# Kernel tuning notes

Hardware: AMD Instinct MI355X
Metric: run time of the kernel (lower is better)

## Reference

```python
import jax, jax.numpy as jnp
import numpy as np

SIDE = 64; EMB = 16; CH = 64; K = 64; V = 64; L = 8
N = SIDE * SIDE

def _pos_table(side, d):
    pe = np.array([[p / np.power(10000, 2 * (j // 2) / d) for j in range(d)]
                   if p != 0 else np.zeros(d) for p in range(side)])
    pe[1:, 0::2] = np.sin(pe[1:, 0::2])
    pe[1:, 1::2] = np.cos(pe[1:, 1::2])
    return pe.astype(np.float32)  # [side, d]

def _pos_emb():
    # Replicates torch .view(1, emb, side, 1): plain reshape of [side, emb] -> [emb, side]
    t = _pos_table(SIDE, EMB).reshape(EMB, SIDE)
    xe = np.broadcast_to(t[:, :, None], (EMB, SIDE, SIDE))
    ye = np.broadcast_to(t[:, None, :], (EMB, SIDE, SIDE))
    return jnp.asarray(np.concatenate([xe, ye], 0).reshape(1, 2 * EMB, N))

def _conv_mask():
    # CausalConv mask, see_center=False, 5x5: zero center pixel onward in center row, and all rows below
    m = np.ones((CH, 3, 5, 5), np.float32)
    m[:, :, 2, 2:] = 0.0
    m[:, :, 3:, :] = 0.0
    return jnp.asarray(m)

def _lrelu(x):
    return jnp.where(x >= 0, x, 0.01 * x)  # LeakyReLU(0.01)

def _bn(x, g, b, eps=1e-5):
    # training-mode batch norm (biased variance), channel axis = 1
    axes = (0,) + tuple(range(2, x.ndim))
    m = jnp.mean(x, axes, keepdims=True)
    var = jnp.mean((x - m) ** 2, axes, keepdims=True)
    sh = (1, -1) + (1,) * (x.ndim - 2)
    return g.reshape(sh) * (x - m) / jnp.sqrt(var + eps) + b.reshape(sh)

def _cv1(w, b, x):
    # 1x1 Conv1d: [O,I] x [B,I,N] -> [B,O,N]
    return jnp.einsum('oi,bin->bon', w, x) + b[:, None]

def reference(x, conv_w, conv_b, bn0_g, bn0_b, q_w, q_b, fk_w, fk_b, ck_w, ck_b,
              fv_w, fv_b, cv_w, cv_b, bn_g, bn_b, out_w, out_b):
    B = x.shape[0]
    pos = jnp.broadcast_to(_pos_emb(), (B, 2 * EMB, N))
    mask = jnp.tril(jnp.ones((N, N), jnp.float32))

    # masked causal conv input layer + BN + LeakyReLU
    w = conv_w * _conv_mask()
    h = jax.lax.conv_general_dilated(x, w, (1, 1), [(2, 2), (2, 2)],
                                     dimension_numbers=('NCHW', 'OIHW', 'NCHW'))
    h = h + conv_b[None, :, None, None]
    h = _lrelu(_bn(h, bn0_g, bn0_b)).reshape(B, CH, N)

    k0 = jnp.zeros((B, K, N), x.dtype)
    v0 = jnp.zeros((B, V, N), x.dtype)
    inv_sqrt_k = 1.0 / jnp.sqrt(jnp.float32(K))

    def layer(carry, p):
        h, k, v = carry
        qw, qb, fkw, fkb, ckw, ckb, fvw, fvb, cvw, cvb, g, bb = p
        x0 = jnp.concatenate([h, pos], 1)            # [B, CH+32, N]
        x0k = jnp.concatenate([x0, k], 1)            # [B, 160, N]
        x0v = jnp.concatenate([x0, v], 1)
        fk = jax.nn.sigmoid(_cv1(fkw, fkb, x0k))
        ck = _lrelu(_cv1(ckw, ckb, x0k))
        k_new = fk * k + ck                          # highway-gated persistent K
        fv = jax.nn.sigmoid(_cv1(fvw, fvb, x0v))
        cv_ = _lrelu(_cv1(cvw, cvb, x0v))
        v_new = fv * v + cv_
        q = _lrelu(_cv1(qw, qb, x0))                 # [B, K, N]
        attn = jnp.einsum('bkn,bkm->bnm', q, k) * inv_sqrt_k  # uses OLD k
        attn = attn * mask + (1.0 - mask) * (-10000.0)
        attn = jax.nn.softmax(attn, axis=-1) * mask
        out1 = jnp.einsum('bnm,bvm->bvn', attn, v)   # uses OLD v; [B, V, N]
        # original code computes fc(out1) but discards it (out2 overwritten)
        h2 = _lrelu(_bn(out1, g, bb))
        return (h2, k_new, v_new), None

    params = (q_w, q_b, fk_w, fk_b, ck_w, ck_b, fv_w, fv_b, cv_w, cv_b, bn_g, bn_b)
    (h, k, v), _ = jax.lax.scan(layer, (h, k0, v0), params)

    out = jnp.einsum('oi,bin->bon', out_w, h) + out_b[None, :, None]
    return out.reshape(B, out_w.shape[0], SIDE, SIDE)

def setup_inputs() -> dict:
    key = jax.random.key(0)
    ks = jax.random.split(key, 12)
    s = 0.05
    return {
        'x': jax.random.normal(ks[0], (2, 3, 64, 64), jnp.float32),
        'conv_w': jax.random.normal(ks[1], (CH, 3, 5, 5), jnp.float32) * s,
        'conv_b': jnp.zeros((CH,), jnp.float32),
        'bn0_g': jnp.ones((CH,), jnp.float32),
        'bn0_b': jnp.zeros((CH,), jnp.float32),
        'q_w': jax.random.normal(ks[2], (L, K, CH + 2 * EMB), jnp.float32) * s,
        'q_b': jnp.zeros((L, K), jnp.float32),
        'fk_w': jax.random.normal(ks[3], (L, K, CH + K + 2 * EMB), jnp.float32) * s,
        'fk_b': jnp.zeros((L, K), jnp.float32),
        'ck_w': jax.random.normal(ks[4], (L, K, CH + K + 2 * EMB), jnp.float32) * s,
        'ck_b': jnp.zeros((L, K), jnp.float32),
        'fv_w': jax.random.normal(ks[5], (L, V, CH + V + 2 * EMB), jnp.float32) * s,
        'fv_b': jnp.zeros((L, V), jnp.float32),
        'cv_w': jax.random.normal(ks[6], (L, V, CH + V + 2 * EMB), jnp.float32) * s,
        'cv_b': jnp.zeros((L, V), jnp.float32),
        'bn_g': jnp.ones((L, CH), jnp.float32),
        'bn_b': jnp.zeros((L, CH), jnp.float32),
        'out_w': jax.random.normal(ks[7], (100, V), jnp.float32) * s,
        'out_b': jnp.zeros((100,), jnp.float32),
    }
```

## Files before the change

### kernel.cpp

```cpp
#include <hip/hip_runtime.h>

#define NPIX 4096
#define CHN  64

typedef __attribute__((ext_vector_type(8))) short short8;
typedef __attribute__((ext_vector_type(8))) unsigned short ushort8;
typedef __attribute__((ext_vector_type(4))) unsigned short ushort4v;
typedef __attribute__((ext_vector_type(4))) float f32x4;

__device__ __forceinline__ float lrelu_(float x){ return x >= 0.f ? x : 0.01f*x; }

__device__ __forceinline__ unsigned short f2bf(float x){
  union { float f; unsigned u; } v; v.f = x;
  unsigned r = v.u + 0x7FFF + ((v.u >> 16) & 1);
  return (unsigned short)(r >> 16);
}
__device__ __forceinline__ float bf2f(unsigned short h){
  union { unsigned u; float f; } v; v.u = ((unsigned)h) << 16;
  return v.f;
}

__global__ void pos_kernel(float* __restrict__ pos){
  int idx = blockIdx.x*256 + threadIdx.x;
  int c = idx >> 12;
  int n = idx & (NPIX-1);
  int bcoord = (c < 16) ? (n >> 6) : (n & 63);
  int a = (c < 16) ? c : (c - 16);
  int flat = a*64 + bcoord;
  int p = flat >> 4;
  int j = flat & 15;
  float val = 0.f;
  if (p != 0){
    float ex = (float)(j & ~1) * (1.f/16.f);
    float w = powf(10000.f, -ex);
    float ang = (float)p * w;
    val = (j & 1) ? cosf(ang) : sinf(ang);
  }
  pos[idx] = val;
}

__global__ void wtr_kernel(const float* __restrict__ qw, const float* __restrict__ fkw,
                           const float* __restrict__ ckw, const float* __restrict__ fvw,
                           const float* __restrict__ cvw, float* __restrict__ wt){
  int idx = blockIdx.x*256 + threadIdx.x;
  if (idx >= 376832) return;
  if (idx < 49152){
    int l = idx / 6144, r = idx % 6144, i = r >> 6, o = r & 63;
    wt[idx] = qw[(l*64 + o)*96 + i];
  } else {
    int e = idx - 49152;
    int mat = e / 81920, r = e % 81920;
    int l = r / 10240, rr = r % 10240, i = rr >> 6, o = rr & 63;
    const float* src = (mat==0) ? fkw : (mat==1) ? ckw : (mat==2) ? fvw : cvw;
    wt[idx] = src[(l*64 + o)*160 + i];
  }
}

__global__ void conv_in_kernel(const float* __restrict__ x, const float* __restrict__ cw,
                               const float* __restrict__ cb, float* __restrict__ out){
  int b = blockIdx.x >> 6;
  int o = blockIdx.x & 63;
  float w[3][12];
  #pragma unroll
  for (int ci=0; ci<3; ++ci){
    const float* wp = cw + (o*3+ci)*25;
    #pragma unroll
    for (int tt=0; tt<10; ++tt) w[ci][tt] = wp[tt];
    w[ci][10] = wp[10]; w[ci][11] = wp[11];
  }
  float bias = cb[o];
  for (int px = threadIdx.x; px < NPIX; px += 256){
    int y = px >> 6, xx = px & 63;
    float acc = bias;
    #pragma unroll
    for (int ci=0; ci<3; ++ci){
      const float* xp = x + ((b*3+ci)<<12);
      #pragma unroll
      for (int ky=0; ky<3; ++ky){
        int yy = y + ky - 2;
        if (yy < 0) continue;
        int nk = (ky==2) ? 2 : 5;
        #pragma unroll
        for (int kx=0; kx<5; ++kx){
          if (kx >= nk) break;
          int xc = xx + kx - 2;
          if (xc < 0 || xc > 63) continue;
          acc += xp[(yy<<6) + xc] * w[ci][ky*5+kx];
        }
      }
    }
    out[(b*CHN+o)*NPIX + px] = acc;
  }
}

__global__ __launch_bounds__(1024) void bn_stats_kernel(const float* __restrict__ xin,
                                                        float* __restrict__ stats){
  int c = blockIdx.x;
  int t = threadIdx.x;
  float s = 0.f, ss = 0.f;
  #pragma unroll
  for (int it=0; it<8; ++it){
    int idx = t + it*1024;
    float v = xin[(((idx>>12))*CHN + c)*NPIX + (idx & (NPIX-1))];
    s += v; ss += v*v;
  }
  #pragma unroll
  for (int o=1; o<64; o<<=1){ s += __shfl_xor(s,o); ss += __shfl_xor(ss,o); }
  __shared__ float ps[16], pq[16];
  if ((t & 63) == 0){ ps[t>>6] = s; pq[t>>6] = ss; }
  __syncthreads();
  if (t == 0){
    float S=0.f, Q=0.f;
    #pragma unroll
    for (int i=0;i<16;++i){ S += ps[i]; Q += pq[i]; }
    float mu = S*(1.f/8192.f);
    float var = Q*(1.f/8192.f) - mu*mu;
    var = fmaxf(var, 0.f);
    stats[c*2]   = mu;
    stats[c*2+1] = rsqrtf(var + 1e-5f);
  }
}

__global__ void bn_apply_kernel(const float* __restrict__ xin, const float* __restrict__ stats,
                                const float* __restrict__ g, const float* __restrict__ bb,
                                float* __restrict__ hout){
  int idx = blockIdx.x*256 + threadIdx.x;
  int e = idx << 2;
  int c = (e >> 12) & 63;
  float mu = stats[c*2], rstd = stats[c*2+1];
  float gain = g[c]*rstd;
  float beta = bb[c] - gain*mu;
  float4 v = *(const float4*)(xin + e);
  float4 r;
  r.x = lrelu_(gain*v.x + beta);
  r.y = lrelu_(gain*v.y + beta);
  r.z = lrelu_(gain*v.z + beta);
  r.w = lrelu_(gain*v.w + beta);
  *(float4*)(hout + e) = r;
}

__global__ __launch_bounds__(256) void cv1_kernel(
    const float* __restrict__ hbuf, const float* __restrict__ pos,
    const float* __restrict__ kold, const float* __restrict__ vold,
    const float* __restrict__ qwt,
    const float* __restrict__ fkwt, const float* __restrict__ ckwt,
    const float* __restrict__ fvwt, const float* __restrict__ cvwt,
    const float* __restrict__ qbi,  const float* __restrict__ fkb,
    const float* __restrict__ ckb,  const float* __restrict__ fvb,
    const float* __restrict__ cvb,
    unsigned short* __restrict__ qh, unsigned short* __restrict__ ql,
    float* __restrict__ knew, unsigned short* __restrict__ khn, unsigned short* __restrict__ kln,
    float* __restrict__ vnew, unsigned short* __restrict__ vhTn, unsigned short* __restrict__ vlTn)
{
  int t = threadIdx.x;
  int o  = t & 63;
  int wv = t >> 6;
  int b    = blockIdx.x >> 8;
  int tile = blockIdx.x & 255;
  int n0 = tile*16 + wv*4;

  const float* hb = hbuf + b*CHN*NPIX + n0;
  const float* kb = kold + b*CHN*NPIX + n0;
  const float* vb = vold + b*CHN*NPIX + n0;
  const float* pb = pos + n0;

  auto load4 = [&](const float* p, float* dst){
    float4 a = *(const float4*)p;
    dst[0]=a.x; dst[1]=a.y; dst[2]=a.z; dst[3]=a.w;
  };

  float x[4];
  long obase = (long)(b*CHN+o)*NPIX + n0;
  size_t nbase = ((size_t)b*NPIX + n0)*64 + o;

  {
    float aq[4];
    float bias = qbi[o];
    #pragma unroll
    for (int j=0;j<4;++j) aq[j]=bias;
    #pragma unroll 4
    for (int i=0;i<64;++i){
      load4(hb + i*NPIX, x);
      float w = qwt[i*64 + o];
      #pragma unroll
      for (int j=0;j<4;++j) aq[j] += w*x[j];
    }
    #pragma unroll 4
    for (int i=0;i<32;++i){
      load4(pb + i*NPIX, x);
      float w = qwt[(64+i)*64 + o];
      #pragma unroll
      for (int j=0;j<4;++j) aq[j] += w*x[j];
    }
    #pragma unroll
    for (int j=0;j<4;++j){
      float v = lrelu_(aq[j]) * 0.125f;
      unsigned short hb16 = f2bf(v);
      qh[nbase + (size_t)j*64] = hb16;
      ql[nbase + (size_t)j*64] = f2bf(v - bf2f(hb16));
    }
  }

  {
    float af[4], ac[4];
    float bf = fkb[o], bc = ckb[o];
    #pragma unroll
    for (int j=0;j<4;++j){ af[j]=bf; ac[j]=bc; }
    #pragma unroll 4
    for (int i=0;i<64;++i){
      load4(hb + i*NPIX, x);
      float wf = fkwt[i*64+o], wc = ckwt[i*64+o];
      #pragma unroll
      for (int j=0;j<4;++j){ af[j] += wf*x[j]; ac[j] += wc*x[j]; }
    }
    #pragma unroll 4
    for (int i=0;i<32;++i){
      load4(pb + i*NPIX, x);
      float wf = fkwt[(64+i)*64+o], wc = ckwt[(64+i)*64+o];
      #pragma unroll
      for (int j=0;j<4;++j){ af[j] += wf*x[j]; ac[j] += wc*x[j]; }
    }
    #pragma unroll 4
    for (int i=0;i<64;++i){
      load4(kb + i*NPIX, x);
      float wf = fkwt[(96+i)*64+o], wc = ckwt[(96+i)*64+o];
      #pragma unroll
      for (int j=0;j<4;++j){ af[j] += wf*x[j]; ac[j] += wc*x[j]; }
    }
    float kv[4];
    load4(kb + o*NPIX, kv);
    #pragma unroll
    for (int j=0;j<4;++j){
      float fk = 1.f/(1.f+__expf(-af[j]));
      float kn = fk*kv[j] + lrelu_(ac[j]);
      knew[obase+j] = kn;
      unsigned short hb16 = f2bf(kn);
      khn[nbase + (size_t)j*64] = hb16;
      kln[nbase + (size_t)j*64] = f2bf(kn - bf2f(hb16));
    }
  }

  {
    float af[4], ac[4];
    float bf = fvb[o], bc = cvb[o];
    #pragma unroll
    for (int j=0;j<4;++j){ af[j]=bf; ac[j]=bc; }
    #pragma unroll 4
    for (int i=0;i<64;++i){
      load4(hb + i*NPIX, x);
      float wf = fvwt[i*64+o], wc = cvwt[i*64+o];
      #pragma unroll
      for (int j=0;j<4;++j){ af[j] += wf*x[j]; ac[j] += wc*x[j]; }
    }
    #pragma unroll 4
    for (int i=0;i<32;++i){
      load4(pb + i*NPIX, x);
      float wf = fvwt[(64+i)*64+o], wc = cvwt[(64+i)*64+o];
      #pragma unroll
      for (int j=0;j<4;++j){ af[j] += wf*x[j]; ac[j] += wc*x[j]; }
    }
    #pragma unroll 4
    for (int i=0;i<64;++i){
      load4(vb + i*NPIX, x);
      float wf = fvwt[(96+i)*64+o], wc = cvwt[(96+i)*64+o];
      #pragma unroll
      for (int j=0;j<4;++j){ af[j] += wf*x[j]; ac[j] += wc*x[j]; }
    }
    float vv[4];
    load4(vb + o*NPIX, vv);
    ushort4v vph, vpl;
    #pragma unroll
    for (int j=0;j<4;++j){
      float fv = 1.f/(1.f+__expf(-af[j]));
      float vn = fv*vv[j] + lrelu_(ac[j]);
      vnew[obase+j] = vn;
      unsigned short hb16 = f2bf(vn);
      vph[j] = hb16;
      vpl[j] = f2bf(vn - bf2f(hb16));
    }
    *(ushort4v*)(vhTn + ((size_t)(b*CHN+o))*NPIX + n0) = vph;
    *(ushort4v*)(vlTn + ((size_t)(b*CHN+o))*NPIX + n0) = vpl;
  }
}

__global__ __launch_bounds__(128) void attn_mfma(
    const unsigned short* __restrict__ qhg, const unsigned short* __restrict__ qlg,
    const unsigned short* __restrict__ khg, const unsigned short* __restrict__ klg,
    const unsigned short* __restrict__ vhg, const unsigned short* __restrict__ vlg,
    float* __restrict__ part)
{
  int bid = 639 - (int)blockIdx.x;
  int b = 0, id = bid;
  if (id >= 320){ b = 1; id -= 320; }
  int pidx = bid;
  int rem = id, k = 0;
  while (rem >= 32*(k+1)){ rem -= 32*(k+1); ++k; }
  int rt    = 32*k + rem/(k+1);
  int chunk = rem - (rem/(k+1))*(k+1);

  int C0  = chunk << 10;
  int end = min(C0 + 1024, rt*32 + 32);
  int nt  = (end - C0 + 63) >> 6;

  int t = threadIdx.x;
  int w = t >> 6;
  int l = t & 63;
  int r = l & 15;
  int g = l >> 4;
  int n_g = rt*32 + w*16 + r;

  __shared__ __align__(16) char KH[8192], KL[8192];
  __shared__ __align__(16) char VH[8192], VL[8192];
  __shared__ __align__(16) char PH[2][2048], PL[2][2048];

  const unsigned short* qhp = qhg + (size_t)b*NPIX*64;
  const unsigned short* qlp = qlg + (size_t)b*NPIX*64;
  const unsigned short* khp = khg + (size_t)b*NPIX*64;
  const unsigned short* klp = klg + (size_t)b*NPIX*64;
  const unsigned short* vhp = vhg + (size_t)b*CHN*NPIX;
  const unsigned short* vlp = vlg + (size_t)b*CHN*NPIX;

  short8 qh0 = *(const short8*)(qhp + (size_t)n_g*64 + 8*g);
  short8 qh1 = *(const short8*)(qhp + (size_t)n_g*64 + 8*g + 32);
  short8 ql0 = *(const short8*)(qlp + (size_t)n_g*64 + 8*g);
  short8 ql1 = *(const short8*)(qlp + (size_t)n_g*64 + 8*g + 32);

  f32x4 zero4 = {0.f,0.f,0.f,0.f};
  f32x4 oacc[4];
  #pragma unroll
  for (int vf=0; vf<4; ++vf) oacc[vf] = zero4;
  float m_run = -1e30f, l_run = 0.f;

  int nmax_w = rt*32 + w*16 + 15;

  for (int ti=0; ti<nt; ++ti){
    int m0 = C0 + (ti<<6);
    __syncthreads();
    #pragma unroll
    for (int p=0; p<4; ++p){
      int slot = t + (p<<7);
      int row = slot >> 3, cc = slot & 7;
      int off = row*128 + ((cc ^ (row & 7)) << 4);
      *(ushort8*)(KH + off) = *(const ushort8*)(khp + (size_t)(m0+row)*64 + cc*8);
      *(ushort8*)(KL + off) = *(const ushort8*)(klp + (size_t)(m0+row)*64 + cc*8);
      *(ushort8*)(VH + off) = *(const ushort8*)(vhp + (size_t)row*NPIX + m0 + cc*8);
      *(ushort8*)(VL + off) = *(const ushort8*)(vlp + (size_t)row*NPIX + m0 + cc*8);
    }
    __syncthreads();

    if (m0 <= nmax_w){
      f32x4 sf[4];
      #pragma unroll
      for (int mf=0; mf<4; ++mf) sf[mf] = zero4;
      #pragma unroll
      for (int kc=0; kc<2; ++kc){
        short8 qfh = kc ? qh1 : qh0;
        short8 qfl = kc ? ql1 : ql0;
        int ch = ((g + 4*kc) ^ (r & 7)) << 4;
        #pragma unroll
        for (int mf=0; mf<4; ++mf){
          int ro = (16*mf + r)*128;
          short8 ah = *(const short8*)(KH + ro + ch);
          short8 al = *(const short8*)(KL + ro + ch);
          sf[mf] = __builtin_amdgcn_mfma_f32_16x16x32_bf16(ah, qfh, sf[mf], 0,0,0);
          sf[mf] = __builtin_amdgcn_mfma_f32_16x16x32_bf16(al, qfh, sf[mf], 0,0,0);
          sf[mf] = __builtin_amdgcn_mfma_f32_16x16x32_bf16(ah, qfl, sf[mf], 0,0,0);
        }
      }
      float pv[16];
      float mx = -1e30f;
      #pragma unroll
      for (int mf=0; mf<4; ++mf){
        #pragma unroll
        for (int q2=0; q2<4; ++q2){
          int mg = m0 + 16*mf + 4*g + q2;
          float s = sf[mf][q2];
          s = (mg <= n_g) ? s : -1e30f;
          pv[mf*4+q2] = s;
          mx = fmaxf(mx, s);
        }
      }
      mx = fmaxf(mx, __shfl_xor(mx, 16));
      mx = fmaxf(mx, __shfl_xor(mx, 32));
      float m_new = fmaxf(m_run, mx);
      float alpha = __expf(m_run - m_new);
      float ps = 0.f;
      #pragma unroll
      for (int i=0; i<16; ++i){ pv[i] = __expf(pv[i] - m_new); ps += pv[i]; }
      ps += __shfl_xor(ps, 16);
      ps += __shfl_xor(ps, 32);
      l_run = l_run*alpha + ps;
      m_run = m_new;

      #pragma unroll
      for (int mf=0; mf<4; ++mf){
        unsigned short h_[4], l_[4];
        #pragma unroll
        for (int q2=0; q2<4; ++q2){
          float xv = pv[mf*4+q2];
          h_[q2] = f2bf(xv);
          l_[q2] = f2bf(xv - bf2f(h_[q2]));
        }
        int addr = r*128 + ((((g>>1) + 2*mf) ^ (r & 7)) << 4) + ((g&1)<<3);
        uint2 wh = make_uint2((unsigned)h_[0] | ((unsigned)h_[1]<<16),
                              (unsigned)h_[2] | ((unsigned)h_[3]<<16));
        uint2 wl = make_uint2((unsigned)l_[0] | ((unsigned)l_[1]<<16),
                              (unsigned)l_[2] | ((unsigned)l_[3]<<16));
        *(uint2*)(PH[w] + addr) = wh;
        *(uint2*)(PL[w] + addr) = wl;
      }
      #pragma unroll
      for (int vf=0; vf<4; ++vf) oacc[vf] *= alpha;

      #pragma unroll
      for (int kc=0; kc<2; ++kc){
        int ch = ((g + 4*kc) ^ (r & 7)) << 4;
        short8 pfh = *(const short8*)(PH[w] + r*128 + ch);
        short8 pfl = *(const short8*)(PL[w] + r*128 + ch);
        #pragma unroll
        for (int vf=0; vf<4; ++vf){
          int ro = (16*vf + r)*128;
          short8 ah = *(const short8*)(VH + ro + ch);
          short8 al = *(const short8*)(VL + ro + ch);
          oacc[vf] = __builtin_amdgcn_mfma_f32_16x16x32_bf16(ah, pfh, oacc[vf], 0,0,0);
          oacc[vf] = __builtin_amdgcn_mfma_f32_16x16x32_bf16(al, pfh, oacc[vf], 0,0,0);
          oacc[vf] = __builtin_amdgcn_mfma_f32_16x16x32_bf16(ah, pfl, oacc[vf], 0,0,0);
        }
      }
    }
  }

  float* pacc = part + (size_t)pidx * 2112;
  int nl = w*16 + r;
  #pragma unroll
  for (int vf=0; vf<4; ++vf)
    *(f32x4*)(pacc + nl*64 + 16*vf + 4*g) = oacc[vf];
  if (g == 0){
    pacc[2048 + nl*2]   = m_run;
    pacc[2048 + nl*2+1] = l_run;
  }
}

__global__ __launch_bounds__(256) void attn_combine(const float* __restrict__ part,
                                                    float* __restrict__ out1){
  int bid = blockIdx.x;
  int b = bid >> 7, rt = bid & 127;
  int k = rt >> 5;
  int nch = k + 1;
  int base = b*320 + 16*k*(k+1) + (rt - 32*k)*nch;

  int t = threadIdx.x;
  int nl = t & 31, vq = t >> 5;

  float M = -1e30f;
  #pragma unroll
  for (int c=0; c<4; ++c)
    if (c < nch) M = fmaxf(M, part[(size_t)(base+c)*2112 + 2048 + nl*2]);

  float L = 0.f;
  float val[8];
  #pragma unroll
  for (int jj=0; jj<8; ++jj) val[jj] = 0.f;
  #pragma unroll
  for (int c=0; c<4; ++c){
    if (c < nch){
      const float* pa = part + (size_t)(base+c)*2112;
      float wgt = __expf(pa[2048 + nl*2] - M);
      L += pa[2048 + nl*2 + 1] * wgt;
      #pragma unroll
      for (int jj=0; jj<8; ++jj) val[jj] += wgt * pa[nl*64 + vq*8 + jj];
    }
  }
  float invL = 1.f / L;
  #pragma unroll
  for (int jj=0; jj<8; ++jj)
    out1[((size_t)b*CHN + vq*8 + jj)*NPIX + rt*32 + nl] = val[jj]*invL;
}

__global__ __launch_bounds__(256) void final_kernel(const float* __restrict__ h,
                                                    const float* __restrict__ ow,
                                                    const float* __restrict__ ob,
                                                    float* __restrict__ out){
  int idx = blockIdx.x*256 + threadIdx.x;
  int b  = idx / 409600;
  int r  = idx - b*409600;
  int oc = r >> 12;
  int n  = r & (NPIX-1);
  const float* hp = h + (size_t)b*CHN*NPIX + n;
  const float* wp = ow + oc*64;
  float acc = ob[oc];
  #pragma unroll
  for (int v=0; v<64; ++v) acc += wp[v]*hp[(size_t)v*NPIX];
  out[idx] = acc;
}

extern "C" void kernel_launch(void* const* d_in, const int* in_sizes, int n_in,
                              void* d_out, int out_size, void* d_ws, size_t ws_size,
                              hipStream_t stream){
  const float* x     = (const float*)d_in[0];
  const float* convw = (const float*)d_in[1];
  const float* convb = (const float*)d_in[2];
  const float* bn0g  = (const float*)d_in[3];
  const float* bn0b  = (const float*)d_in[4];
  const float* qw    = (const float*)d_in[5];
  const float* qbias = (const float*)d_in[6];
  const float* fkw   = (const float*)d_in[7];
  const float* fkb   = (const float*)d_in[8];
  const float* ckw   = (const float*)d_in[9];
  const float* ckb   = (const float*)d_in[10];
  const float* fvw   = (const float*)d_in[11];
  const float* fvb   = (const float*)d_in[12];
  const float* cvw   = (const float*)d_in[13];
  const float* cvb   = (const float*)d_in[14];
  const float* bng   = (const float*)d_in[15];
  const float* bnb   = (const float*)d_in[16];
  const float* ow    = (const float*)d_in[17];
  const float* ob    = (const float*)d_in[18];

  const size_t TEN = (size_t)2*CHN*NPIX;
  const size_t BFU = TEN/2;
  float* ws   = (float*)d_ws;
  float* pos  = ws;
  float* h    = pos + 32*NPIX;
  float* k0   = h  + TEN;
  float* k1   = k0 + TEN;
  float* v0   = k1 + TEN;
  float* v1   = v0 + TEN;
  float* o1   = v1 + TEN;
  float* stats = o1 + TEN;
  float* wt   = stats + 128;
  float* bfb  = wt + 376832;
  unsigned short* qh  = (unsigned short*)(bfb);
  unsigned short* ql  = (unsigned short*)(bfb + BFU);
  unsigned short* kh0 = (unsigned short*)(bfb + 2*BFU);
  unsigned short* kh1 = (unsigned short*)(bfb + 3*BFU);
  unsigned short* kl0 = (unsigned short*)(bfb + 4*BFU);
  unsigned short* kl1 = (unsigned short*)(bfb + 5*BFU);
  unsigned short* vh0 = (unsigned short*)(bfb + 6*BFU);
  unsigned short* vh1 = (unsigned short*)(bfb + 7*BFU);
  unsigned short* vl0 = (unsigned short*)(bfb + 8*BFU);
  unsigned short* vl1 = (unsigned short*)(bfb + 9*BFU);
  float* part = bfb + 10*BFU;

  hipMemsetAsync(k0, 0, TEN*sizeof(float), stream);
  hipMemsetAsync(v0, 0, TEN*sizeof(float), stream);
  hipMemsetAsync(kh0, 0, TEN*2, stream);
  hipMemsetAsync(kl0, 0, TEN*2, stream);
  hipMemsetAsync(vh0, 0, TEN*2, stream);
  hipMemsetAsync(vl0, 0, TEN*2, stream);

  pos_kernel<<<512,256,0,stream>>>(pos);
  wtr_kernel<<<1472,256,0,stream>>>(qw, fkw, ckw, fvw, cvw, wt);
  conv_in_kernel<<<128,256,0,stream>>>(x, convw, convb, o1);
  bn_stats_kernel<<<64,1024,0,stream>>>(o1, stats);
  bn_apply_kernel<<<512,256,0,stream>>>(o1, stats, bn0g, bn0b, h);

  float* kfp[2] = {k0,k1};
  float* vfp[2] = {v0,v1};
  unsigned short* khb[2] = {kh0,kh1};
  unsigned short* klb[2] = {kl0,kl1};
  unsigned short* vhb[2] = {vh0,vh1};
  unsigned short* vlb[2] = {vl0,vl1};
  for (int l=0; l<8; ++l){
    float* kold = kfp[l&1]; float* knew = kfp[(l+1)&1];
    float* vold = vfp[l&1]; float* vnew = vfp[(l+1)&1];
    cv1_kernel<<<512,256,0,stream>>>(h, pos, kold, vold,
        wt + l*6144,
        wt + 49152 + l*10240,
        wt + 49152 + 81920 + l*10240,
        wt + 49152 + 2*81920 + l*10240,
        wt + 49152 + 3*81920 + l*10240,
        qbias + l*64, fkb + l*64, ckb + l*64, fvb + l*64, cvb + l*64,
        qh, ql,
        knew, khb[(l+1)&1], klb[(l+1)&1],
        vnew, vhb[(l+1)&1], vlb[(l+1)&1]);
    attn_mfma<<<640,128,0,stream>>>(qh, ql, khb[l&1], klb[l&1], vhb[l&1], vlb[l&1], part);
    attn_combine<<<256,256,0,stream>>>(part, o1);
    bn_stats_kernel<<<64,1024,0,stream>>>(o1, stats);
    bn_apply_kernel<<<512,256,0,stream>>>(o1, stats, bng + l*64, bnb + l*64, h);
  }
  final_kernel<<<3200,256,0,stream>>>(h, ow, ob, (float*)d_out);
}
```

Before: 869.2 us.

## Fuse BN stats into attention combine, prefetch attention tiles, parallelize input conv

Three separate changes. First, attn_combine now emits per-block partial sums and squared sums per channel, and a new bn_apply2 kernel reduces them, removing the separate bn_stats pass over o1 in every layer. Second, attn_mfma register-prefetches the next K/V tile from global memory while the current tile is being computed, overlapping load latency with MFMA work. Third, the input convolution weights are transposed in wtr_kernel and conv_in is launched with many more blocks, one pixel per thread group. The variance is now computed as E[x^2]-mu^2, which is less numerically robust than the two-pass form, and the prefetch adds register pressure.

```diff
diff --git a/kernel.cpp b/kernel.cpp
--- a/kernel.cpp
+++ b/kernel.cpp
@@ -41,56 +41,57 @@
 
 __global__ void wtr_kernel(const float* __restrict__ qw, const float* __restrict__ fkw,
                            const float* __restrict__ ckw, const float* __restrict__ fvw,
-                           const float* __restrict__ cvw, float* __restrict__ wt){
+                           const float* __restrict__ cvw, const float* __restrict__ convw,
+                           float* __restrict__ wt){
   int idx = blockIdx.x*256 + threadIdx.x;
-  if (idx >= 376832) return;
+  if (idx >= 381632) return;
   if (idx < 49152){
     int l = idx / 6144, r = idx % 6144, i = r >> 6, o = r & 63;
     wt[idx] = qw[(l*64 + o)*96 + i];
-  } else {
+  } else if (idx < 376832){
     int e = idx - 49152;
     int mat = e / 81920, r = e % 81920;
     int l = r / 10240, rr = r % 10240, i = rr >> 6, o = rr & 63;
     const float* src = (mat==0) ? fkw : (mat==1) ? ckw : (mat==2) ? fvw : cvw;
     wt[idx] = src[(l*64 + o)*160 + i];
-  }
-}
-
-__global__ void conv_in_kernel(const float* __restrict__ x, const float* __restrict__ cw,
-                               const float* __restrict__ cb, float* __restrict__ out){
-  int b = blockIdx.x >> 6;
-  int o = blockIdx.x & 63;
-  float w[3][12];
+  } else {
+    int e = idx - 376832;
+    int o = e & 63, tap = e >> 6;
+    int ci = tap / 25, r = tap % 25;
+    wt[idx] = convw[(o*3 + ci)*25 + r];
+  }
+}
+
+__global__ __launch_bounds__(256) void conv_in_kernel(const float* __restrict__ x,
+                                                      const float* __restrict__ cwt,
+                                                      const float* __restrict__ cb,
+                                                      float* __restrict__ out){
+  int t = threadIdx.x;
+  int o = t & 63;
+  int sub = t >> 6;
+  int bid = blockIdx.x;
+  int b = bid >> 10;
+  int n = ((bid & 1023) << 2) + sub;
+  int y = n >> 6, xx = n & 63;
+  float acc = cb[o];
   #pragma unroll
   for (int ci=0; ci<3; ++ci){
-    const float* wp = cw + (o*3+ci)*25;
-    #pragma unroll
-    for (int tt=0; tt<10; ++tt) w[ci][tt] = wp[tt];
-    w[ci][10] = wp[10]; w[ci][11] = wp[11];
-  }
-  float bias = cb[o];
-  for (int px = threadIdx.x; px < NPIX; px += 256){
-    int y = px >> 6, xx = px & 63;
-    float acc = bias;
-    #pragma unroll
-    for (int ci=0; ci<3; ++ci){
-      const float* xp = x + ((b*3+ci)<<12);
-      #pragma unroll
-      for (int ky=0; ky<3; ++ky){
-        int yy = y + ky - 2;
-        if (yy < 0) continue;
-        int nk = (ky==2) ? 2 : 5;
-        #pragma unroll
-        for (int kx=0; kx<5; ++kx){
-          if (kx >= nk) break;
-          int xc = xx + kx - 2;
-          if (xc < 0 || xc > 63) continue;
-          acc += xp[(yy<<6) + xc] * w[ci][ky*5+kx];
-        }
+    const float* xp = x + ((b*3+ci)<<12);
+    #pragma unroll
+    for (int ky=0; ky<3; ++ky){
+      int yy = y + ky - 2;
+      if (yy < 0) continue;
+      int nk = (ky==2) ? 2 : 5;
+      #pragma unroll
+      for (int kx=0; kx<5; ++kx){
+        if (kx >= nk) break;
+        int xc = xx + kx - 2;
+        if (xc < 0 || xc > 63) continue;
+        acc += xp[(yy<<6) + xc] * cwt[(ci*25 + ky*5 + kx)*64 + o];
       }
     }
-    out[(b*CHN+o)*NPIX + px] = acc;
-  }
+  }
+  out[(b*CHN+o)*NPIX + n] = acc;
 }
 
 __global__ __launch_bounds__(1024) void bn_stats_kernel(const float* __restrict__ xin,
@@ -137,6 +138,39 @@
   r.z = lrelu_(gain*v.z + beta);
   r.w = lrelu_(gain*v.w + beta);
   *(float4*)(hout + e) = r;
+}
+
+__global__ __launch_bounds__(256) void bn_apply2_kernel(const float* __restrict__ xin,
+                                                        const float* __restrict__ psum,
+                                                        const float* __restrict__ psq,
+                                                        const float* __restrict__ g,
+                                                        const float* __restrict__ bb,
+                                                        float* __restrict__ hout){
+  int bid = blockIdx.x;
+  int ebase = bid << 10;
+  int c = (ebase >> 12) & 63;
+  int t = threadIdx.x;
+  float s = psum[c*256 + t];
+  float q = psq[c*256 + t];
+  #pragma unroll
+  for (int o=1; o<64; o<<=1){ s += __shfl_xor(s,o); q += __shfl_xor(q,o); }
+  __shared__ float as[4], aq[4];
+  if ((t & 63) == 0){ as[t>>6] = s; aq[t>>6] = q; }
+  __syncthreads();
+  float S = as[0]+as[1]+as[2]+as[3];
+  float Q = aq[0]+aq[1]+aq[2]+aq[3];
+  float mu = S*(1.f/8192.f);
+  float var = fmaxf(Q*(1.f/8192.f) - mu*mu, 0.f);
+  float rstd = rsqrtf(var + 1e-5f);
+  float gain = g[c]*rstd;
+  float beta = bb[c] - gain*mu;
+  float4 v = *(const float4*)(xin + ebase + t*4);
+  float4 r;
+  r.x = lrelu_(gain*v.x + beta);
+  r.y = lrelu_(gain*v.y + beta);
+  r.z = lrelu_(gain*v.z + beta);
+  r.w = lrelu_(gain*v.w + beta);
+  *(float4*)(hout + ebase + t*4) = r;
 }
 
 __global__ __launch_bounds__(256) void cv1_kernel(
@@ -325,6 +359,26 @@
   short8 ql0 = *(const short8*)(qlp + (size_t)n_g*64 + 8*g);
   short8 ql1 = *(const short8*)(qlp + (size_t)n_g*64 + 8*g + 32);
 
+  int srow[4], scc8[4], soff[4];
+  #pragma unroll
+  for (int p=0; p<4; ++p){
+    int slot = t + (p<<7);
+    int row = slot >> 3, cc = slot & 7;
+    srow[p] = row; scc8[p] = cc*8;
+    soff[p] = row*128 + ((cc ^ (row & 7)) << 4);
+  }
+
+  ushort8 rkh[4], rkl[4], rvh[4], rvl[4];
+  auto issue = [&](int m0){
+    #pragma unroll
+    for (int p=0; p<4; ++p){
+      rkh[p] = *(const ushort8*)(khp + (size_t)(m0+srow[p])*64 + scc8[p]);
+      rkl[p] = *(const ushort8*)(klp + (size_t)(m0+srow[p])*64 + scc8[p]);
+      rvh[p] = *(const ushort8*)(vhp + (size_t)srow[p]*NPIX + m0 + scc8[p]);
+      rvl[p] = *(const ushort8*)(vlp + (size_t)srow[p]*NPIX + m0 + scc8[p]);
+    }
+  };
+
   f32x4 zero4 = {0.f,0.f,0.f,0.f};
   f32x4 oacc[4];
   #pragma unroll
@@ -333,20 +387,19 @@
 
   int nmax_w = rt*32 + w*16 + 15;
 
+  issue(C0);
   for (int ti=0; ti<nt; ++ti){
     int m0 = C0 + (ti<<6);
     __syncthreads();
     #pragma unroll
     for (int p=0; p<4; ++p){
-      int slot = t + (p<<7);
-      int row = slot >> 3, cc = slot & 7;
-      int off = row*128 + ((cc ^ (row & 7)) << 4);
-      *(ushort8*)(KH + off) = *(const ushort8*)(khp + (size_t)(m0+row)*64 + cc*8);
-      *(ushort8*)(KL + off) = *(const ushort8*)(klp + (size_t)(m0+row)*64 + cc*8);
-      *(ushort8*)(VH + off) = *(const ushort8*)(vhp + (size_t)row*NPIX + m0 + cc*8);
-      *(ushort8*)(VL + off) = *(const ushort8*)(vlp + (size_t)row*NPIX + m0 + cc*8);
+      *(ushort8*)(KH + soff[p]) = rkh[p];
+      *(ushort8*)(KL + soff[p]) = rkl[p];
+      *(ushort8*)(VH + soff[p]) = rvh[p];
+      *(ushort8*)(VL + soff[p]) = rvl[p];
     }
     __syncthreads();
+    if (ti+1 < nt) issue(m0 + 64);
 
     if (m0 <= nmax_w){
       f32x4 sf[4];
@@ -442,7 +495,9 @@
 }
 
 __global__ __launch_bounds__(256) void attn_combine(const float* __restrict__ part,
-                                                    float* __restrict__ out1){
+                                                    float* __restrict__ out1,
+                                                    float* __restrict__ psum,
+                                                    float* __restrict__ psq){
   int bid = blockIdx.x;
   int b = bid >> 7, rt = bid & 127;
   int k = rt >> 5;
@@ -472,9 +527,29 @@
     }
   }
   float invL = 1.f / L;
-  #pragma unroll
-  for (int jj=0; jj<8; ++jj)
-    out1[((size_t)b*CHN + vq*8 + jj)*NPIX + rt*32 + nl] = val[jj]*invL;
+  float s[8], q[8];
+  #pragma unroll
+  for (int jj=0; jj<8; ++jj){
+    float v = val[jj]*invL;
+    out1[((size_t)b*CHN + vq*8 + jj)*NPIX + rt*32 + nl] = v;
+    s[jj] = v; q[jj] = v*v;
+  }
+  #pragma unroll
+  for (int o2=1; o2<32; o2<<=1){
+    #pragma unroll
+    for (int jj=0; jj<8; ++jj){
+      s[jj] += __shfl_xor(s[jj], o2);
+      q[jj] += __shfl_xor(q[jj], o2);
+    }
+  }
+  if (nl == 0){
+    #pragma unroll
+    for (int jj=0; jj<8; ++jj){
+      int c = vq*8 + jj;
+      psum[c*256 + bid] = s[jj];
+      psq [c*256 + bid] = q[jj];
+    }
+  }
 }
 
 __global__ __launch_bounds__(256) void final_kernel(const float* __restrict__ h,
@@ -528,8 +603,10 @@
   float* v1   = v0 + TEN;
   float* o1   = v1 + TEN;
   float* stats = o1 + TEN;
-  float* wt   = stats + 128;
-  float* bfb  = wt + 376832;
+  float* psum = stats + 128;
+  float* psq  = psum + 64*256;
+  float* wt   = psq + 64*256;
+  float* bfb  = wt + 381632;
   unsigned short* qh  = (unsigned short*)(bfb);
   unsigned short* ql  = (unsigned short*)(bfb + BFU);
   unsigned short* kh0 = (unsigned short*)(bfb + 2*BFU);
@@ -550,8 +627,8 @@
   hipMemsetAsync(vl0, 0, TEN*2, stream);
 
   pos_kernel<<<512,256,0,stream>>>(pos);
-  wtr_kernel<<<1472,256,0,stream>>>(qw, fkw, ckw, fvw, cvw, wt);
-  conv_in_kernel<<<128,256,0,stream>>>(x, convw, convb, o1);
+  wtr_kernel<<<1491,256,0,stream>>>(qw, fkw, ckw, fvw, cvw, convw, wt);
+  conv_in_kernel<<<2048,256,0,stream>>>(x, wt + 376832, convb, o1);
   bn_stats_kernel<<<64,1024,0,stream>>>(o1, stats);
   bn_apply_kernel<<<512,256,0,stream>>>(o1, stats, bn0g, bn0b, h);
 
@@ -575,9 +652,8 @@
         knew, khb[(l+1)&1], klb[(l+1)&1],
         vnew, vhb[(l+1)&1], vlb[(l+1)&1]);
     attn_mfma<<<640,128,0,stream>>>(qh, ql, khb[l&1], klb[l&1], vhb[l&1], vlb[l&1], part);
-    attn_combine<<<256,256,0,stream>>>(part, o1);
-    bn_stats_kernel<<<64,1024,0,stream>>>(o1, stats);
-    bn_apply_kernel<<<512,256,0,stream>>>(o1, stats, bng + l*64, bnb + l*64, h);
+    attn_combine<<<256,256,0,stream>>>(part, o1, psum, psq);
+    bn_apply2_kernel<<<512,256,0,stream>>>(o1, psum, psq, bng + l*64, bnb + l*64, h);
   }
   final_kernel<<<3200,256,0,stream>>>(h, ow, ob, (float*)d_out);
 }
```

Measured after the change: 823.0 us. 1.06x faster.
